# Kernel optimization log

Hardware: AMD Instinct MI355X
Metric: run time of the kernel (lower is better)

The kernel has to match this reference:

```python
import jax, jax.numpy as jnp
import numpy as np
import math

# Spherical conv per Esteves et al. spherical CNNs (sph_conv_batch):
#   1) spherical-harmonic transform of input on an n x n equiangular grid
#   2) per-degree multiply by zonal filter coeffs w[c_in, l, c_out],
#      scaled by 2*pi*sqrt(4*pi/(2l+1))
#   3) inverse transform, plus bias add.
# Implemented as FFT over longitude + Legendre quadrature over colatitude.

BATCH, N_GRID, C_IN, C_OUT = 64, 32, 128, 128
L_MAX = N_GRID // 2  # spherical-harmonic bandwidth


def _legendre_Q(L, n):
    """Normalized associated Legendre N_lm * P_l^m(cos theta_j).
    Returns Q (L, 2L-1, n) with m index offset by L-1, and theta (n,)."""
    theta = np.pi * (np.arange(n) + 0.5) / n
    x, sx = np.cos(theta), np.sin(theta)
    P = np.zeros((L, L, n))
    P[0, 0] = 1.0
    for m in range(1, L):
        P[m, m] = -(2 * m - 1) * sx * P[m - 1, m - 1]
    for m in range(L - 1):
        P[m + 1, m] = (2 * m + 1) * x * P[m, m]
        for l in range(m + 2, L):
            P[l, m] = ((2 * l - 1) * x * P[l - 1, m] - (l + m - 1) * P[l - 2, m]) / (l - m)
    Q = np.zeros((L, 2 * L - 1, n))
    for l in range(L):
        for m in range(l + 1):
            Nlm = np.sqrt((2 * l + 1) / (4 * np.pi)
                          * np.exp(math.lgamma(l - m + 1) - math.lgamma(l + m + 1)))
            Q[l, L - 1 + m] = Nlm * P[l, m]
            Q[l, L - 1 - m] = ((-1) ** m) * Nlm * P[l, m]
    return Q, theta


def _sph_conv(inputs, weights, bias):
    b, n, _, c_in = inputs.shape
    L = weights.shape[1]
    Q, theta = _legendre_Q(L, n)
    # quadrature: sin(theta)*dtheta*dphi, dtheta = pi/n, dphi = 2*pi/n
    wj = np.sin(theta) * (np.pi / n) * (2.0 * np.pi / n)
    Qw = jnp.asarray(Q * wj, dtype=jnp.float32).astype(jnp.complex64)   # (L, 2L-1, n)
    Qs = jnp.asarray(Q, dtype=jnp.float32).astype(jnp.complex64)
    ms = np.arange(-(L - 1), L) % n  # 2L-1 distinct FFT bins
    # forward SHT: FFT over phi then Legendre quadrature over theta
    F = jnp.fft.fft(inputs.astype(jnp.complex64), axis=2)[:, :, ms, :]  # (b, n, 2L-1, c_in)
    coef = jnp.einsum('lmj,bjmc->blmc', Qw, F)                          # (b, L, 2L-1, c_in)
    # zonal spectral filter: per-degree scale 2*pi*sqrt(4*pi/(2l+1))
    scale = jnp.asarray(2.0 * np.pi * np.sqrt(4.0 * np.pi / (2.0 * np.arange(L) + 1.0)),
                        jnp.float32)
    chat = jnp.einsum('blmi,ilo->blmo', coef, weights.astype(jnp.complex64))
    chat = chat * scale[None, :, None, None]
    # inverse SHT: Legendre synthesis then inverse FFT over phi
    G = jnp.einsum('blmo,lmj->bjmo', chat, Qs)                          # (b, n, 2L-1, c_out)
    Gfull = jnp.zeros((b, n, n, G.shape[-1]), jnp.complex64).at[:, :, ms, :].set(G)
    out = jnp.real(jnp.fft.ifft(Gfull, axis=2)) * n                    # (b, n, n, c_out)
    return out + bias


def setup_inputs() -> dict:
    key = jax.random.key(0)
    k1, k2 = jax.random.split(key)
    std = 2.0 / (2.0 * np.pi * np.sqrt(L_MAX * C_IN))
    inputs = jax.random.normal(k1, (BATCH, N_GRID, N_GRID, C_IN), jnp.float32)
    weights = jax.random.normal(k2, (C_IN, L_MAX, C_OUT), jnp.float32) * std
    bias = jnp.zeros((1, 1, 1, C_OUT), jnp.float32)
    return {"inputs": inputs, "weights": weights, "bias": bias}


def reference(inputs, weights, bias):
    return _sph_conv(inputs, weights, bias)
```

## Files before the change

kernel.cpp:

```cpp
#include <hip/hip_runtime.h>
#include <hip/hip_bf16.h>
#include <math.h>


#define NPAIR 136
#define PADC 140

typedef __attribute__((ext_vector_type(8))) short short8;
typedef __attribute__((ext_vector_type(4))) float f32x4;
#define MFMA16(A, B, C) __builtin_amdgcn_mfma_f32_16x16x32_bf16(A, B, C, 0, 0, 0)

static __device__ __forceinline__ float us2f(unsigned int u) {
  union { unsigned int i; float f; } v; v.i = u << 16; return v.f;
}
static __device__ __forceinline__ unsigned short f2us(float f) {
  __hip_bfloat16 h = __float2bfloat16(f);
  return *(unsigned short*)&h;
}
static __device__ __forceinline__ float lo_f(unsigned int pk) {
  union { unsigned int i; float f; } v; v.i = pk << 16; return v.f;
}
static __device__ __forceinline__ float hi_f(unsigned int pk) {
  union { unsigned int i; float f; } v; v.i = pk & 0xffff0000u; return v.f;
}
static __device__ __forceinline__ unsigned int packbf(float a, float b) {
  return (unsigned int)f2us(a) | ((unsigned int)f2us(b) << 16);
}

__device__ __align__(16) unsigned short g_atab_h[NPAIR * 32];
__device__ __align__(16) float          g_stab[32 * PADC];
__device__ int g_tab_ready;

static __device__ __forceinline__ int detect_fp32(const void* xin) {
  const unsigned short* u = (const unsigned short*)xin;
  int lane = threadIdx.x & 63;
  int big = 0;
#pragma unroll
  for (int q = 0; q < 4; ++q) {
    float v = us2f((unsigned int)u[lane * 8 + q * 2]);
    if (!(fabsf(v) <= 1e3f)) big = 1;
  }
  unsigned long long mask = __ballot(big);
  return (__popcll(mask) >= 16) ? 1 : 0;
}

#define DEF_TRIG \
  constexpr float CT[32] = { \
    1.0f, 0.98078528f, 0.92387953f, 0.83146961f, 0.70710678f, 0.55557023f, \
    0.38268343f, 0.19509032f, 0.0f, -0.19509032f, -0.38268343f, -0.55557023f, \
    -0.70710678f, -0.83146961f, -0.92387953f, -0.98078528f, -1.0f, \
    -0.98078528f, -0.92387953f, -0.83146961f, -0.70710678f, -0.55557023f, \
    -0.38268343f, -0.19509032f, 0.0f, 0.19509032f, 0.38268343f, 0.55557023f, \
    0.70710678f, 0.83146961f, 0.92387953f, 0.98078528f }; \
  constexpr float ST[32] = { \
    0.0f, 0.19509032f, 0.38268343f, 0.55557023f, 0.70710678f, 0.83146961f, \
    0.92387953f, 0.98078528f, 1.0f, 0.98078528f, 0.92387953f, 0.83146961f, \
    0.70710678f, 0.55557023f, 0.38268343f, 0.19509032f, 0.0f, \
    -0.19509032f, -0.38268343f, -0.55557023f, -0.70710678f, -0.83146961f, \
    -0.92387953f, -0.98078528f, -1.0f, -0.98078528f, -0.92387953f, \
    -0.83146961f, -0.70710678f, -0.55557023f, -0.38268343f, -0.19509032f }

__global__ void k_init() {
  if (g_tab_ready) return;
  const int pair = blockIdx.x, j = threadIdx.x;
  int m = 0;
#pragma unroll
  for (int mm = 1; mm < 16; ++mm) {
    int off = mm * 16 - (mm * (mm - 1)) / 2;
    if (off <= pair) m = mm;
  }
  const int l = m + (pair - (m * 16 - (m * (m - 1)) / 2));
  double theta = M_PI * (j + 0.5) / 32.0;
  double x = cos(theta), sx = sin(theta);
  double wj = sx * (M_PI / 32.0) * (2.0 * M_PI / 32.0);
  double pmm = 1.0;
  for (int k = 1; k <= m; ++k) pmm *= -(2.0 * k - 1.0) * sx;
  double p = pmm, pl1 = 0.0, pl2 = 0.0;
  for (int ll = m; ll <= l; ++ll) {
    if (ll == m)          p = pmm;
    else if (ll == m + 1) p = (2.0 * m + 1.0) * x * pmm;
    else                  p = ((2.0 * ll - 1.0) * x * pl1 - (double)(ll + m - 1) * pl2) / (double)(ll - m);
    pl2 = pl1; pl1 = p;
  }
  double r = 1.0;
  for (int k = l - m + 1; k <= l + m; ++k) r *= (double)k;
  double Nlm = sqrt((2.0 * l + 1.0) / (4.0 * M_PI) / r);
  g_atab_h[pair * 32 + j] = f2us((float)(Nlm * p * wj));
  g_stab[j * PADC + pair] = (float)(Nlm * p * (2.0 * M_PI * sqrt(4.0 * M_PI / (2.0 * l + 1.0)))
                                    * (m ? 2.0 : 1.0));
  if (pair == NPAIR - 1 && j == 31) g_tab_ready = 1;
}

__global__ __launch_bounds__(256) void k_fwd(const void* __restrict__ xin,
                                             unsigned int* __restrict__ ws) {
  const int fp32m = detect_fp32(xin);
  __shared__ __align__(16) unsigned short xs[32 * 264];
  __shared__ __align__(16) unsigned int   fsp[128 * 36];
  const int blk = blockIdx.x;
  const int b = (blk & 7) | (((blk >> 7) & 7) << 3);
  const int cq = (blk >> 3) & 15;
  const int t = threadIdx.x;
  uint4 at0 = ((const uint4*)g_atab_h)[t];
  uint4 at1 = ((const uint4*)g_atab_h)[t + 256];
  uint4 at2;
  if (t < 32) at2 = ((const uint4*)g_atab_h)[512 + t];
  if (fp32m) {
    const float* xf = (const float*)xin;
#pragma unroll
    for (int it = 0; it < 8; ++it) {
      int i = t + it * 256;
      int s = i >> 1, hf = i & 1;
      float4 v = *(const float4*)(xf + ((size_t)b * 1024 + s) * 128 + cq * 8 + hf * 4);
      int p = s & 31, j = s >> 5;
      *(uint2*)&xs[p * 264 + j * 8 + hf * 4] = make_uint2(packbf(v.x, v.y), packbf(v.z, v.w));
    }
  } else {
    const unsigned short* xh = (const unsigned short*)xin;
#pragma unroll
    for (int it = 0; it < 4; ++it) {
      int s = t + it * 256;
      uint4 v = *(const uint4*)(xh + ((size_t)b * 1024 + s) * 128 + cq * 8);
      int p = s & 31, j = s >> 5;
      *(uint4*)&xs[p * 264 + j * 8] = v;
    }
  }
  __syncthreads();
  {
    DEF_TRIG;
    const int j = t >> 3, c = t & 7, rb = j * 8 + c;
    float x0  = us2f((unsigned int)xs[rb]);
    float x16 = us2f((unsigned int)xs[16 * 264 + rb]);
    float sp[16], dm[16];
#pragma unroll
    for (int p = 1; p <= 15; ++p) {
      float a  = us2f((unsigned int)xs[p * 264 + rb]);
      float bq = us2f((unsigned int)xs[(32 - p) * 264 + rb]);
      sp[p] = a + bq; dm[p] = a - bq;
    }
#pragma unroll
    for (int mi = 0; mi < 16; ++mi) {
      float re = x0 + ((mi & 1) ? -x16 : x16);
      float im = 0.f;
#pragma unroll
      for (int p = 1; p <= 15; ++p) {
        re += sp[p] * CT[(mi * p) & 31];
        im -= dm[p] * ST[(mi * p) & 31];
      }
      fsp[(mi * 8 + c) * 36 + j] = packbf(re, im);
    }
  }
  __syncthreads();
  ((uint4*)xs)[t] = at0;
  ((uint4*)xs)[t + 256] = at1;
  if (t < 32) ((uint4*)xs)[512 + t] = at2;
  __syncthreads();
  {
    const int m = t >> 4, c = (t >> 1) & 7, jh = t & 1;
    const int cg = cq * 8 + c;
    const int base = m * 16 - (m * (m - 1)) / 2;
    uint4 F[4];
#pragma unroll
    for (int q = 0; q < 4; ++q)
      F[q] = *(const uint4*)&fsp[(m * 8 + c) * 36 + jh * 16 + q * 4];
    for (int l = m; l < 16; ++l) {
      int pair = base + (l - m);
      float sr = 0.f, si = 0.f;
#pragma unroll
      for (int q = 0; q < 2; ++q) {
        uint4 a = ((const uint4*)xs)[pair * 4 + jh * 2 + q];
        float a0 = us2f(a.x & 0xffff), a1 = us2f(a.x >> 16);
        float a2 = us2f(a.y & 0xffff), a3 = us2f(a.y >> 16);
        float a4 = us2f(a.z & 0xffff), a5 = us2f(a.z >> 16);
        float a6 = us2f(a.w & 0xffff), a7 = us2f(a.w >> 16);
        uint4 f0 = F[2 * q], f1 = F[2 * q + 1];
        sr += a0 * lo_f(f0.x) + a1 * lo_f(f0.y) + a2 * lo_f(f0.z) + a3 * lo_f(f0.w)
            + a4 * lo_f(f1.x) + a5 * lo_f(f1.y) + a6 * lo_f(f1.z) + a7 * lo_f(f1.w);
        si += a0 * hi_f(f0.x) + a1 * hi_f(f0.y) + a2 * hi_f(f0.z) + a3 * hi_f(f0.w)
            + a4 * hi_f(f1.x) + a5 * hi_f(f1.y) + a6 * hi_f(f1.z) + a7 * hi_f(f1.w);
      }
      sr += __shfl_xor(sr, 1, 64);
      si += __shfl_xor(si, 1, 64);
      if (jh == 0)
        ws[((size_t)b * NPAIR + pair) * 128 + cg] = packbf(sr, si);
    }
  }
}

__global__ __launch_bounds__(1024, 4) void k_cb(const unsigned int* __restrict__ ws,
                                                char* __restrict__ outbuf,
                                                const void* __restrict__ Wv,
                                                const void* __restrict__ biasv,
                                                const void* __restrict__ xin) {
  const int fp32m = detect_fp32(xin);
  __shared__ __align__(16) unsigned int chs[32 * PADC];
  __shared__ __align__(16) float        stb[32 * PADC];
  const int b = blockIdx.x >> 2, oq = blockIdx.x & 3;
  const int t = threadIdx.x;
  for (int i = t; i < 32 * PADC / 4; i += 1024)
    ((float4*)stb)[i] = ((const float4*)g_stab)[i];
  {
    const int lw = t >> 6, lane = t & 63;
    const int col = lane & 15, quad = lane >> 4;
    const int s = col;
    const int av = (s <= lw);
    const int pv = av ? (s * 16 - (s * (s - 1)) / 2 + (lw - s)) : 0;
    short8 Bf[2][4];
    if (fp32m) {
      const float* Wf = (const float*)Wv;
#pragma unroll
      for (int nt = 0; nt < 2; ++nt) {
        const float* wp = Wf + (size_t)lw * 128 + oq * 32 + nt * 16 + col;
#pragma unroll
        for (int kc = 0; kc < 4; ++kc)
#pragma unroll
          for (int r = 0; r < 8; ++r)
            ((unsigned short*)&Bf[nt][kc])[r] =
                f2us(wp[(size_t)(kc * 32 + quad * 8 + r) * 2048]);
      }
    } else {
      const unsigned short* Wh = (const unsigned short*)Wv;
#pragma unroll
      for (int nt = 0; nt < 2; ++nt) {
        const unsigned short* wp = Wh + (size_t)lw * 128 + oq * 32 + nt * 16 + col;
#pragma unroll
        for (int kc = 0; kc < 4; ++kc)
#pragma unroll
          for (int r = 0; r < 8; ++r)
            ((unsigned short*)&Bf[nt][kc])[r] = wp[(size_t)(kc * 32 + quad * 8 + r) * 2048];
      }
    }
    f32x4 aR0 = {0.f, 0.f, 0.f, 0.f}, aI0 = aR0, aR1 = aR0, aI1 = aR0;
#pragma unroll
    for (int kc = 0; kc < 4; ++kc) {
      uint4 u0 = {0u, 0u, 0u, 0u}, u1 = u0;
      if (av) {
        const unsigned int* cp = ws + ((size_t)b * NPAIR + pv) * 128 + kc * 32 + quad * 8;
        u0 = *(const uint4*)cp;
        u1 = *(const uint4*)(cp + 4);
      }
      short8 Ar, Ai;
      Ar[0] = (short)(u0.x & 0xffff); Ai[0] = (short)(u0.x >> 16);
      Ar[1] = (short)(u0.y & 0xffff); Ai[1] = (short)(u0.y >> 16);
      Ar[2] = (short)(u0.z & 0xffff); Ai[2] = (short)(u0.z >> 16);
      Ar[3] = (short)(u0.w & 0xffff); Ai[3] = (short)(u0.w >> 16);
      Ar[4] = (short)(u1.x & 0xffff); Ai[4] = (short)(u1.x >> 16);
      Ar[5] = (short)(u1.y & 0xffff); Ai[5] = (short)(u1.y >> 16);
      Ar[6] = (short)(u1.z & 0xffff); Ai[6] = (short)(u1.z >> 16);
      Ar[7] = (short)(u1.w & 0xffff); Ai[7] = (short)(u1.w >> 16);
      aR0 = MFMA16(Ar, Bf[0][kc], aR0);
      aI0 = MFMA16(Ai, Bf[0][kc], aI0);
      aR1 = MFMA16(Ar, Bf[1][kc], aR1);
      aI1 = MFMA16(Ai, Bf[1][kc], aI1);
    }
#pragma unroll
    for (int reg = 0; reg < 4; ++reg) {
      int slot = quad * 4 + reg;
      if (slot <= lw) {
        int pp_ = slot * 16 - (slot * (slot - 1)) / 2 + (lw - slot);
        chs[(0 * 16 + col) * PADC + pp_] = packbf(aR0[reg], aI0[reg]);
        chs[(1 * 16 + col) * PADC + pp_] = packbf(aR1[reg], aI1[reg]);
      }
    }
  }
  const int j = t >> 5, ol = t & 31;
  const int o = oq * 32 + ol;
  const float bv = fp32m ? ((const float*)biasv)[o]
                         : us2f((unsigned int)((const unsigned short*)biasv)[o]);
  __syncthreads();

  float Gr[16], Gi[16];
#pragma unroll
  for (int mm = 0; mm < 16; ++mm) { Gr[mm] = 0.f; Gi[mm] = 0.f; }
  {
    float4 s4 = {0.f, 0.f, 0.f, 0.f};
    uint4  c4 = {0u, 0u, 0u, 0u};
    int pair = 0;
#pragma unroll
    for (int mm = 0; mm < 16; ++mm) {
#pragma unroll
      for (int l = mm; l < 16; ++l) {
        if ((pair & 3) == 0) {
          s4 = *(const float4*)&stb[j * PADC + pair];
          c4 = *(const uint4*)&chs[ol * PADC + pair];
        }
        const int r = pair & 3;
        const float        s  = (r == 0) ? s4.x : (r == 1) ? s4.y : (r == 2) ? s4.z : s4.w;
        const unsigned int cv = (r == 0) ? c4.x : (r == 1) ? c4.y : (r == 2) ? c4.z : c4.w;
        Gr[mm] += s * lo_f(cv);
        Gi[mm] += s * hi_f(cv);
        ++pair;
      }
    }
  }
  DEF_TRIG;
#pragma unroll
  for (int pp = 0; pp <= 16; ++pp) {
    float A = 0.f, Bv = 0.f;
#pragma unroll
    for (int mm = 0; mm < 16; ++mm) {
      A  += Gr[mm] * CT[(mm * pp) & 31];
      Bv += Gi[mm] * ST[(mm * pp) & 31];
    }
    const int p2 = (32 - pp) & 31;
    size_t e1 = (size_t)b * 131072 + (size_t)(j * 32 + pp) * 128 + o;
    size_t e2 = (size_t)b * 131072 + (size_t)(j * 32 + p2) * 128 + o;
    if (fp32m) {
      *(float*)(outbuf + e1 * 4) = bv + A - Bv;
      *(float*)(outbuf + e2 * 4) = bv + A + Bv;
    } else {
      *(unsigned short*)(outbuf + e1 * 2) = f2us(bv + A - Bv);
      *(unsigned short*)(outbuf + e2 * 2) = f2us(bv + A + Bv);
    }
  }
}

extern "C" void kernel_launch(void* const* d_in, const int* in_sizes, int n_in,
                              void* d_out, int out_size, void* d_ws, size_t ws_size,
                              hipStream_t stream) {
  const void* xin  = d_in[0];
  const void* W    = d_in[1];
  const void* bias = d_in[2];
  char* out = (char*)d_out;
  unsigned int* ws = (unsigned int*)d_ws;

  hipLaunchKernelGGL(k_init, dim3(NPAIR), dim3(32),   0, stream);
  hipLaunchKernelGGL(k_fwd,  dim3(1024),  dim3(256),  0, stream, xin, ws);
  hipLaunchKernelGGL(k_cb,   dim3(256),   dim3(1024), 0, stream, ws, out, W, bias, xin);
}
```

Before: 114.3 us.

## Use MFMA for forward Legendre quadrature and pre-transpose weights into workspace

The forward Legendre step in k_fwd now runs as one bf16 16x16x32 MFMA per m-order instead of scalar dot products with shuffles. To feed it, real and imaginary FFT outputs are stored as separate bf16 rows in shared memory. k_fwd also transposes and converts the weights into a bf16 layout contiguous in c_in, stored at an offset in the workspace. k_cb can then load its B fragments with vector loads instead of strided scalar gathers. The cost is extra global writes in k_fwd and a dependence on workspace size and layout.

Result: faster. 111.0 us (-2.9%).

```diff
diff --git a/kernel.cpp b/kernel.cpp
--- a/kernel.cpp
+++ b/kernel.cpp
@@ -5,6 +5,7 @@
 
 #define NPAIR 136
 #define PADC 140
+#define WT_OFF (8u << 20)
 
 typedef __attribute__((ext_vector_type(8))) short short8;
 typedef __attribute__((ext_vector_type(4))) float f32x4;
@@ -92,10 +93,11 @@
 }
 
 __global__ __launch_bounds__(256) void k_fwd(const void* __restrict__ xin,
-                                             unsigned int* __restrict__ ws) {
+                                             unsigned int* __restrict__ ws,
+                                             const void* __restrict__ Wv) {
   const int fp32m = detect_fp32(xin);
   __shared__ __align__(16) unsigned short xs[32 * 264];
-  __shared__ __align__(16) unsigned int   fsp[128 * 36];
+  __shared__ __align__(16) unsigned short fsp2[16 * 16 * 36];
   const int blk = blockIdx.x;
   const int b = (blk & 7) | (((blk >> 7) & 7) << 3);
   const int cq = (blk >> 3) & 15;
@@ -104,6 +106,21 @@
   uint4 at1 = ((const uint4*)g_atab_h)[t + 256];
   uint4 at2;
   if (t < 32) at2 = ((const uint4*)g_atab_h)[512 + t];
+  if (blk < 512) {
+    const int loe = blk * 4 + (t >> 6);
+    const int l = loe >> 7, o = loe & 127, c0 = (t & 63) * 2;
+    unsigned int pk;
+    if (fp32m) {
+      const float* Wf = (const float*)Wv;
+      pk = packbf(Wf[(size_t)c0 * 2048 + l * 128 + o],
+                  Wf[(size_t)(c0 + 1) * 2048 + l * 128 + o]);
+    } else {
+      const unsigned short* Wh = (const unsigned short*)Wv;
+      pk = (unsigned int)Wh[(size_t)c0 * 2048 + l * 128 + o]
+         | ((unsigned int)Wh[(size_t)(c0 + 1) * 2048 + l * 128 + o] << 16);
+    }
+    ((unsigned int*)((char*)ws + WT_OFF))[(size_t)loe * 64 + (c0 >> 1)] = pk;
+  }
   if (fp32m) {
     const float* xf = (const float*)xin;
 #pragma unroll
@@ -146,7 +163,8 @@
         re += sp[p] * CT[(mi * p) & 31];
         im -= dm[p] * ST[(mi * p) & 31];
       }
-      fsp[(mi * 8 + c) * 36 + j] = packbf(re, im);
+      fsp2[(mi * 16 + 2 * c + 0) * 36 + j] = f2us(re);
+      fsp2[(mi * 16 + 2 * c + 1) * 36 + j] = f2us(im);
     }
   }
   __syncthreads();
@@ -155,40 +173,32 @@
   if (t < 32) ((uint4*)xs)[512 + t] = at2;
   __syncthreads();
   {
-    const int m = t >> 4, c = (t >> 1) & 7, jh = t & 1;
-    const int cg = cq * 8 + c;
-    const int base = m * 16 - (m * (m - 1)) / 2;
-    uint4 F[4];
-#pragma unroll
-    for (int q = 0; q < 4; ++q)
-      F[q] = *(const uint4*)&fsp[(m * 8 + c) * 36 + jh * 16 + q * 4];
-    for (int l = m; l < 16; ++l) {
-      int pair = base + (l - m);
-      float sr = 0.f, si = 0.f;
-#pragma unroll
-      for (int q = 0; q < 2; ++q) {
-        uint4 a = ((const uint4*)xs)[pair * 4 + jh * 2 + q];
-        float a0 = us2f(a.x & 0xffff), a1 = us2f(a.x >> 16);
-        float a2 = us2f(a.y & 0xffff), a3 = us2f(a.y >> 16);
-        float a4 = us2f(a.z & 0xffff), a5 = us2f(a.z >> 16);
-        float a6 = us2f(a.w & 0xffff), a7 = us2f(a.w >> 16);
-        uint4 f0 = F[2 * q], f1 = F[2 * q + 1];
-        sr += a0 * lo_f(f0.x) + a1 * lo_f(f0.y) + a2 * lo_f(f0.z) + a3 * lo_f(f0.w)
-            + a4 * lo_f(f1.x) + a5 * lo_f(f1.y) + a6 * lo_f(f1.z) + a7 * lo_f(f1.w);
-        si += a0 * hi_f(f0.x) + a1 * hi_f(f0.y) + a2 * hi_f(f0.z) + a3 * hi_f(f0.w)
-            + a4 * hi_f(f1.x) + a5 * hi_f(f1.y) + a6 * hi_f(f1.z) + a7 * hi_f(f1.w);
-      }
-      sr += __shfl_xor(sr, 1, 64);
-      si += __shfl_xor(si, 1, 64);
-      if (jh == 0)
-        ws[((size_t)b * NPAIR + pair) * 128 + cg] = packbf(sr, si);
+    const int wv = t >> 6, lane = t & 63;
+    const int n = lane & 15, quad = lane >> 4;
+    const unsigned short* atab = (const unsigned short*)xs;
+#pragma unroll
+    for (int mi4 = 0; mi4 < 4; ++mi4) {
+      const int mi = wv * 4 + mi4;
+      const int base = mi * 16 - (mi * (mi - 1)) / 2;
+      short8 A = *(const short8*)&atab[(base + n) * 32 + quad * 8];
+      short8 Bv = *(const short8*)&fsp2[(mi * 16 + n) * 36 + quad * 8];
+      f32x4 d = {0.f, 0.f, 0.f, 0.f};
+      d = MFMA16(A, Bv, d);
+#pragma unroll
+      for (int reg = 0; reg < 4; ++reg) {
+        float other = __shfl_xor(d[reg], 1, 64);
+        int slot = quad * 4 + reg;
+        if (!(n & 1) && slot < 16 - mi)
+          ws[((size_t)b * NPAIR + base + slot) * 128 + cq * 8 + (n >> 1)] =
+              packbf(d[reg], other);
+      }
     }
   }
 }
 
 __global__ __launch_bounds__(1024, 4) void k_cb(const unsigned int* __restrict__ ws,
                                                 char* __restrict__ outbuf,
-                                                const void* __restrict__ Wv,
+                                                const unsigned short* __restrict__ wt,
                                                 const void* __restrict__ biasv,
                                                 const void* __restrict__ xin) {
   const int fp32m = detect_fp32(xin);
@@ -205,29 +215,12 @@
     const int av = (s <= lw);
     const int pv = av ? (s * 16 - (s * (s - 1)) / 2 + (lw - s)) : 0;
     short8 Bf[2][4];
-    if (fp32m) {
-      const float* Wf = (const float*)Wv;
-#pragma unroll
-      for (int nt = 0; nt < 2; ++nt) {
-        const float* wp = Wf + (size_t)lw * 128 + oq * 32 + nt * 16 + col;
-#pragma unroll
-        for (int kc = 0; kc < 4; ++kc)
-#pragma unroll
-          for (int r = 0; r < 8; ++r)
-            ((unsigned short*)&Bf[nt][kc])[r] =
-                f2us(wp[(size_t)(kc * 32 + quad * 8 + r) * 2048]);
-      }
-    } else {
-      const unsigned short* Wh = (const unsigned short*)Wv;
-#pragma unroll
-      for (int nt = 0; nt < 2; ++nt) {
-        const unsigned short* wp = Wh + (size_t)lw * 128 + oq * 32 + nt * 16 + col;
-#pragma unroll
-        for (int kc = 0; kc < 4; ++kc)
-#pragma unroll
-          for (int r = 0; r < 8; ++r)
-            ((unsigned short*)&Bf[nt][kc])[r] = wp[(size_t)(kc * 32 + quad * 8 + r) * 2048];
-      }
+#pragma unroll
+    for (int nt = 0; nt < 2; ++nt) {
+      const unsigned short* wp = wt + ((size_t)lw * 128 + oq * 32 + nt * 16 + col) * 128;
+#pragma unroll
+      for (int kc = 0; kc < 4; ++kc)
+        Bf[nt][kc] = *(const short8*)(wp + kc * 32 + quad * 8);
     }
     f32x4 aR0 = {0.f, 0.f, 0.f, 0.f}, aI0 = aR0, aR1 = aR0, aI1 = aR0;
 #pragma unroll
@@ -322,8 +315,9 @@
   const void* bias = d_in[2];
   char* out = (char*)d_out;
   unsigned int* ws = (unsigned int*)d_ws;
+  const unsigned short* wt = (const unsigned short*)((char*)d_ws + WT_OFF);
 
   hipLaunchKernelGGL(k_init, dim3(NPAIR), dim3(32),   0, stream);
-  hipLaunchKernelGGL(k_fwd,  dim3(1024),  dim3(256),  0, stream, xin, ws);
-  hipLaunchKernelGGL(k_cb,   dim3(256),   dim3(1024), 0, stream, ws, out, W, bias, xin);
-}
+  hipLaunchKernelGGL(k_fwd,  dim3(1024),  dim3(256),  0, stream, xin, ws, W);
+  hipLaunchKernelGGL(k_cb,   dim3(256),   dim3(1024), 0, stream, ws, out, wt, bias, xin);
+}
```
